# Kernel optimization log

Measured on AMD Instinct MI355X. Metric: run time of the kernel, lower is better.

Reference implementation:

```python
import jax, jax.numpy as jnp
import numpy as np

N, D, N_CLASSES = 4096, 256, 64
MARGIN = 0.2


def setup_inputs() -> dict:
    key = jax.random.key(0)
    k1, k2 = jax.random.split(key)
    embeddings = jax.random.normal(k1, (N, D), dtype=jnp.float32)
    labels = jax.random.randint(k2, (N,), 0, N_CLASSES)
    same = labels[:, None] == labels[None, :]
    eye = jnp.eye(N, dtype=bool)
    return {
        "embeddings": embeddings,
        "positives_mask": same & ~eye,
        "negatives_mask": ~same,
    }


def reference(embeddings, positives_mask, negatives_mask):
    # Pairwise squared L2 distances (LpDistance, normalize_embeddings=False)
    sq = jnp.sum(embeddings * embeddings, axis=1)  # [N]
    d2 = sq[:, None] + sq[None, :] - 2.0 * (embeddings @ embeddings.T)  # [N,N]
    d2 = jnp.maximum(d2, 0.0)

    # Batch-hard mining (argmax/argmin on squared dists == on L2 dists)
    hp = jnp.argmax(jnp.where(positives_mask, d2, -jnp.inf), axis=1)  # hardest positive per anchor
    hn = jnp.argmin(jnp.where(negatives_mask, d2, jnp.inf), axis=1)   # hardest negative per anchor
    rows = jnp.arange(N)

    d_ap = jnp.sqrt(d2[rows, hp])
    d_an = jnp.sqrt(d2[rows, hn])
    d_pn = jnp.sqrt(d2[hp, hn])

    # TripletMarginLoss with swap=True: use min(d(a,n), d(p,n))
    d_an_eff = jnp.minimum(d_an, d_pn)
    l = jax.nn.relu(d_ap - d_an_eff + MARGIN)  # [N] per-anchor triplet loss

    # Only anchors with >=1 positive and >=1 negative form valid triplets
    valid = jnp.any(positives_mask, axis=1) & jnp.any(negatives_mask, axis=1)
    nonzero = (l > 0) & valid
    cnt = jnp.sum(nonzero).astype(jnp.float32)
    total = jnp.sum(jnp.where(nonzero, l, 0.0))
    # AvgNonZeroReducer: mean over strictly-positive losses; 0 if none
    return jnp.where(cnt > 0, total / jnp.maximum(cnt, 1.0), 0.0)
```

## Files before the change

kernel.cpp:

```cpp
#include <hip/hip_runtime.h>
#include <math.h>


#define NN 4096
#define DD 256
#define MARGIN 0.2f
#define NCHUNK 32
#define BK 64

typedef _Float16 f16;
typedef __attribute__((ext_vector_type(8))) _Float16 f16x8;
typedef __attribute__((ext_vector_type(4))) _Float16 f16x4;
typedef __attribute__((ext_vector_type(4))) float f32x4;
typedef unsigned long long u64;
typedef unsigned int u32;

#define OFF_SQ     64
#define OFF_EH     (OFF_SQ + NN * 4)
#define OFF_POSB   (OFF_EH + NN * DD * 2)
#define OFF_PPK    (OFF_POSB + (NN * (long)NN / 8))
#define OFF_PNK    (OFF_PPK + NN * NCHUNK * 8)
#define OFF_LOSS   (OFF_PNK + NN * NCHUNK * 8)

#define CONV_BLOCKS   (NN / 4)
#define REPACK_BLOCKS 4096
#define PREP_BLOCKS   (CONV_BLOCKS + REPACK_BLOCKS)

__device__ __forceinline__ int swz(int r) { return (r ^ (r >> 3)) & 7; }

__device__ __forceinline__ void dma16(const void* g, void* l) {
  __builtin_amdgcn_global_load_lds(
      (const __attribute__((address_space(1))) void*)g,
      (__attribute__((address_space(3))) void*)l, 16, 0, 0);
}

__global__ __launch_bounds__(256)
void prep_kernel(const float* __restrict__ E, const void* __restrict__ pos_raw,
                 f16* __restrict__ Eh, float* __restrict__ sq,
                 u64* __restrict__ posb) {
  const int bid = blockIdx.x;
  const int tid = threadIdx.x;
  if (bid < CONV_BLOCKS) {
    const int row = bid * 4 + (tid >> 6);
    const int lane = tid & 63;
    const float4 v = *(const float4*)&E[(size_t)row * DD + lane * 4];
    f16x4 h;
    h[0] = (f16)v.x; h[1] = (f16)v.y; h[2] = (f16)v.z; h[3] = (f16)v.w;
    *(f16x4*)&Eh[(size_t)row * DD + lane * 4] = h;
    float s = v.x * v.x + v.y * v.y + v.z * v.z + v.w * v.w;
#pragma unroll
    for (int off = 32; off > 0; off >>= 1) s += __shfl_down(s, off);
    if (lane == 0) sq[row] = s;
    return;
  }

  __shared__ int s_ev[4];
  int ev = 0;
#pragma unroll
  for (int k = 0; k < 16; ++k) {
    const int di = tid + (k << 8);
    const u32 v = ((const u32*)pos_raw)[di];
    if (v & 0xffffff00u) ev |= 1;
    if (v == 0x3f800000u) ev |= 2;
    if (di & 1) {
      if (v == 0x3ff00000u) ev |= 4;
      if (v) ev |= 8;
    }
  }
#pragma unroll
  for (int off = 32; off > 0; off >>= 1) ev |= __shfl_xor(ev, off);
  if ((tid & 63) == 0) s_ev[tid >> 6] = ev;
  __syncthreads();
  ev = s_ev[0] | s_ev[1] | s_ev[2] | s_ev[3];
  int f;
  if (ev & 2) f = 2;
  else if (ev & 4) f = 4;
  else if (ev & 1) f = 1;
  else if (ev & 8) f = 0;
  else f = 3;

  const long long stride = (long long)REPACK_BLOCKS * 256;
  const long long base = (long long)(bid - CONV_BLOCKS) * 256 + tid;
#pragma unroll
  for (int it = 0; it < 16; ++it) {
    const long long idx = base + it * stride;
    bool p;
    if (f == 0)      p = ((const u32*)pos_raw)[idx] != 0u;
    else if (f == 1) p = ((const unsigned char*)pos_raw)[idx] != 0;
    else if (f == 2) p = ((const float*)pos_raw)[idx] != 0.f;
    else if (f == 3) p = ((const u64*)pos_raw)[idx] != 0ull;
    else             p = ((const double*)pos_raw)[idx] != 0.0;
    const u64 w = __ballot(p);
    if ((tid & 63) == 0) posb[idx >> 6] = w;
  }
}

__global__ __launch_bounds__(256)
void mine_kernel(const f16* __restrict__ Eh, const float* __restrict__ sq,
                 const u64* __restrict__ posb,
                 u64* __restrict__ part_p, u64* __restrict__ part_n) {
  __shared__ union {
    struct { f16 A[128 * BK]; f16 B[128 * BK]; } t;
    struct { u64 pk[2][128]; u64 nk[2][128]; } r;
  } sm;

  const int tid = threadIdx.x;
  const int lane = tid & 63, wave = tid >> 6;
  const int lx = lane & 15, q = lane >> 4;
  const int wr = wave >> 1, wc = wave & 1;
  const int ib = blockIdx.x & 31, jb = blockIdx.x >> 5;
  const int i0 = ib * 128, j0 = jb * 128;

  f32x4 acc[4][4];
#pragma unroll
  for (int mt = 0; mt < 4; ++mt)
#pragma unroll
    for (int nt = 0; nt < 4; ++nt) acc[mt][nt] = (f32x4)0.f;

  const int drow = lane >> 3;
  const int dslot = lane & 7;

  for (int kk = 0; kk < DD; kk += BK) {
    __syncthreads();
#pragma unroll
    for (int t = 0; t < 4; ++t) {
      const int i = wave * 4 + t;
      const int r = i * 8 + drow;
      const int g = dslot ^ swz(r);
      dma16(Eh + (size_t)(i0 + r) * DD + kk + g * 8, &sm.t.A[i * 512]);
      dma16(Eh + (size_t)(j0 + r) * DD + kk + g * 8, &sm.t.B[i * 512]);
    }
    __syncthreads();
#pragma unroll
    for (int ss = 0; ss < 2; ++ss) {
      f16x8 af[4], bf[4];
#pragma unroll
      for (int mt = 0; mt < 4; ++mt) {
        const int r = wr * 64 + mt * 16 + lx;
        af[mt] = *(const f16x8*)&sm.t.A[r * BK + (((ss * 4 + q) ^ swz(r)) << 3)];
      }
#pragma unroll
      for (int nt = 0; nt < 4; ++nt) {
        const int r = wc * 64 + nt * 16 + lx;
        bf[nt] = *(const f16x8*)&sm.t.B[r * BK + (((ss * 4 + q) ^ swz(r)) << 3)];
      }
#pragma unroll
      for (int mt = 0; mt < 4; ++mt)
#pragma unroll
        for (int nt = 0; nt < 4; ++nt)
          acc[mt][nt] = __builtin_amdgcn_mfma_f32_16x16x32_f16(bf[nt], af[mt], acc[mt][nt], 0, 0, 0);
    }
  }

  float sqi_[4];
  u64 pw_[4], nw_[4];
  const int jw = (j0 + wc * 64) >> 6;
#pragma unroll
  for (int mt = 0; mt < 4; ++mt) {
    const int gi = i0 + wr * 64 + mt * 16 + lx;
    sqi_[mt] = sq[gi];
    const u64 pw = posb[(size_t)gi * (NN / 64) + jw];
    const u64 eye = ((gi >> 6) == jw) ? (1ull << (gi & 63)) : 0ull;
    pw_[mt] = pw;
    nw_[mt] = ~(pw | eye);
  }
  f32x4 sqjv[4];
#pragma unroll
  for (int nt = 0; nt < 4; ++nt)
    sqjv[nt] = *(const f32x4*)&sq[j0 + wc * 64 + nt * 16 + q * 4];
  const u32 jlo_base = ~(u32)(j0 + wc * 64 + q * 4);

  u64 pk[4] = {0ull, 0ull, 0ull, 0ull};
  u64 nk[4] = {0ull, 0ull, 0ull, 0ull};
#pragma unroll
  for (int mt = 0; mt < 4; ++mt) {
#pragma unroll
    for (int nt = 0; nt < 4; ++nt) {
#pragma unroll
      for (int r = 0; r < 4; ++r) {
        const int c = nt * 16 + q * 4 + r;
        const float d2 = fmaxf(fmaf(-2.f, acc[mt][nt][r], sqi_[mt] + sqjv[nt][r]), 0.f);
        const u32 hi = __float_as_uint(d2);
        const u32 lo = jlo_base - (u32)(nt * 16 + r);
        const u64 key = ((u64)hi << 32) | lo;
        const u64 nkey = ((u64)(~hi) << 32) | lo;
        if ((pw_[mt] >> c) & 1ull) pk[mt] = key > pk[mt] ? key : pk[mt];
        if ((nw_[mt] >> c) & 1ull) nk[mt] = nkey > nk[mt] ? nkey : nk[mt];
      }
    }
  }
#pragma unroll
  for (int mt = 0; mt < 4; ++mt) {
#pragma unroll
    for (int off = 16; off < 64; off <<= 1) {
      u64 o = __shfl_xor(pk[mt], off);
      if (o > pk[mt]) pk[mt] = o;
      o = __shfl_xor(nk[mt], off);
      if (o > nk[mt]) nk[mt] = o;
    }
  }

  __syncthreads();
  if (q == 0) {
#pragma unroll
    for (int mt = 0; mt < 4; ++mt) {
      const int lr = wr * 64 + mt * 16 + lx;
      sm.r.pk[wc][lr] = pk[mt];
      sm.r.nk[wc][lr] = nk[mt];
    }
  }
  __syncthreads();
  if (tid < 128) {
    const u64 p0 = sm.r.pk[0][tid], p1 = sm.r.pk[1][tid];
    const u64 n0 = sm.r.nk[0][tid], n1 = sm.r.nk[1][tid];
    part_p[(size_t)jb * NN + i0 + tid] = p0 > p1 ? p0 : p1;
    part_n[(size_t)jb * NN + i0 + tid] = n0 > n1 ? n0 : n1;
  }
}

__global__ __launch_bounds__(256)
void finalize_kernel(const float* __restrict__ E, const float* __restrict__ sq,
                     const u64* __restrict__ part_p, const u64* __restrict__ part_n,
                     float* __restrict__ loss) {
  const int tid = threadIdx.x;
  const int a = blockIdx.x * 4 + (tid >> 6);
  const int lane = tid & 63;
  const int ch = lane & 31;
  u64 key = (lane < 32) ? part_p[(size_t)ch * NN + a] : part_n[(size_t)ch * NN + a];
#pragma unroll
  for (int off = 1; off < 32; off <<= 1) {
    const u64 o = __shfl_xor(key, off);
    if (o > key) key = o;
  }
  const u64 pkey = __shfl(key, 0);
  const u64 nkey = __shfl(key, 32);
  const bool valid = (pkey != 0ull) && (nkey != 0ull);
  const int p = (int)(~(u32)pkey);
  const int n = (int)(~(u32)nkey);
  const int pp = valid ? p : 0, nn = valid ? n : 0;

  const float4 xa = *(const float4*)&E[(size_t)a * DD + lane * 4];
  const float4 xp = *(const float4*)&E[(size_t)pp * DD + lane * 4];
  const float4 xn = *(const float4*)&E[(size_t)nn * DD + lane * 4];
  float dap = xa.x * xp.x + xa.y * xp.y + xa.z * xp.z + xa.w * xp.w;
  float dan = xa.x * xn.x + xa.y * xn.y + xa.z * xn.z + xa.w * xn.w;
  float dpn = xp.x * xn.x + xp.y * xn.y + xp.z * xn.z + xp.w * xn.w;
#pragma unroll
  for (int off = 32; off > 0; off >>= 1) {
    dap += __shfl_down(dap, off);
    dan += __shfl_down(dan, off);
    dpn += __shfl_down(dpn, off);
  }
  if (lane == 0) {
    float l = 0.f;
    if (valid) {
      const float d2ap = fmaxf(sq[a] + sq[pp] - 2.f * dap, 0.f);
      const float d2an = fmaxf(sq[a] + sq[nn] - 2.f * dan, 0.f);
      const float d2pn = fmaxf(sq[pp] + sq[nn] - 2.f * dpn, 0.f);
      l = fmaxf(sqrtf(d2ap) - fminf(sqrtf(d2an), sqrtf(d2pn)) + MARGIN, 0.f);
    }
    loss[a] = l;
  }
}

__global__ __launch_bounds__(1024)
void reduce_kernel(const float* __restrict__ loss, float* __restrict__ out) {
  __shared__ float s_sum[16], s_cnt[16];
  const int tid = threadIdx.x;
  const float4 v = *(const float4*)&loss[tid * 4];
  float s = v.x + v.y + v.z + v.w;
  float c = (v.x > 0.f) + (v.y > 0.f) + (v.z > 0.f) + (v.w > 0.f);
#pragma unroll
  for (int off = 32; off > 0; off >>= 1) {
    s += __shfl_down(s, off);
    c += __shfl_down(c, off);
  }
  if ((tid & 63) == 0) { s_sum[tid >> 6] = s; s_cnt[tid >> 6] = c; }
  __syncthreads();
  if (tid == 0) {
    float ts = 0.f, tc = 0.f;
#pragma unroll
    for (int w = 0; w < 16; ++w) { ts += s_sum[w]; tc += s_cnt[w]; }
    out[0] = (tc > 0.f) ? (ts / fmaxf(tc, 1.f)) : 0.f;
  }
}

extern "C" void kernel_launch(void* const* d_in, const int* in_sizes, int n_in,
                              void* d_out, int out_size, void* d_ws, size_t ws_size,
                              hipStream_t stream) {
  const float* E = (const float*)d_in[0];
  const void* posm = d_in[1];
  float* out = (float*)d_out;
  char* ws = (char*)d_ws;

  float* sq = (float*)(ws + OFF_SQ);
  f16* Eh = (f16*)(ws + OFF_EH);
  u64* posb = (u64*)(ws + OFF_POSB);
  u64* ppk = (u64*)(ws + OFF_PPK);
  u64* pnk = (u64*)(ws + OFF_PNK);
  float* loss = (float*)(ws + OFF_LOSS);

  prep_kernel<<<PREP_BLOCKS, 256, 0, stream>>>(E, posm, Eh, sq, posb);
  mine_kernel<<<32 * NCHUNK, 256, 0, stream>>>(Eh, sq, posb, ppk, pnk);
  finalize_kernel<<<NN / 4, 256, 0, stream>>>(E, sq, ppk, pnk, loss);
  reduce_kernel<<<1, 1024, 0, stream>>>(loss, out);
}
```

Measured before the change: 179.2 us.

## Load GEMM fragments directly from global memory instead of LDS staging

The mine kernel's Gram-matrix GEMM no longer stages 128x64 tiles of A and B into shared memory via global_load_lds with swizzling and barriers. Each wave now reads its MFMA operand fragments straight from global (L2/L1-cached) memory, with the K loop unrolled by two. This removes LDS traffic and the per-K-step barriers and cuts shared memory use, which may raise occupancy. In exchange, each wave issues redundant global loads, since sibling waves re-read the same rows, and it relies on cache hits for data reuse.

Measured after the change: 195.8 us. 9.3% more time.

```diff
diff --git a/kernel.cpp b/kernel.cpp
--- a/kernel.cpp
+++ b/kernel.cpp
@@ -6,7 +6,6 @@
 #define DD 256
 #define MARGIN 0.2f
 #define NCHUNK 32
-#define BK 64
 
 typedef _Float16 f16;
 typedef __attribute__((ext_vector_type(8))) _Float16 f16x8;
@@ -25,14 +24,6 @@
 #define CONV_BLOCKS   (NN / 4)
 #define REPACK_BLOCKS 4096
 #define PREP_BLOCKS   (CONV_BLOCKS + REPACK_BLOCKS)
-
-__device__ __forceinline__ int swz(int r) { return (r ^ (r >> 3)) & 7; }
-
-__device__ __forceinline__ void dma16(const void* g, void* l) {
-  __builtin_amdgcn_global_load_lds(
-      (const __attribute__((address_space(1))) void*)g,
-      (__attribute__((address_space(3))) void*)l, 16, 0, 0);
-}
 
 __global__ __launch_bounds__(256)
 void prep_kernel(const float* __restrict__ E, const void* __restrict__ pos_raw,
@@ -99,10 +90,7 @@
 void mine_kernel(const f16* __restrict__ Eh, const float* __restrict__ sq,
                  const u64* __restrict__ posb,
                  u64* __restrict__ part_p, u64* __restrict__ part_n) {
-  __shared__ union {
-    struct { f16 A[128 * BK]; f16 B[128 * BK]; } t;
-    struct { u64 pk[2][128]; u64 nk[2][128]; } r;
-  } sm;
+  __shared__ u64 s_pk[2][128], s_nk[2][128];
 
   const int tid = threadIdx.x;
   const int lane = tid & 63, wave = tid >> 6;
@@ -117,39 +105,28 @@
 #pragma unroll
     for (int nt = 0; nt < 4; ++nt) acc[mt][nt] = (f32x4)0.f;
 
-  const int drow = lane >> 3;
-  const int dslot = lane & 7;
-
-  for (int kk = 0; kk < DD; kk += BK) {
-    __syncthreads();
-#pragma unroll
-    for (int t = 0; t < 4; ++t) {
-      const int i = wave * 4 + t;
-      const int r = i * 8 + drow;
-      const int g = dslot ^ swz(r);
-      dma16(Eh + (size_t)(i0 + r) * DD + kk + g * 8, &sm.t.A[i * 512]);
-      dma16(Eh + (size_t)(j0 + r) * DD + kk + g * 8, &sm.t.B[i * 512]);
-    }
-    __syncthreads();
-#pragma unroll
-    for (int ss = 0; ss < 2; ++ss) {
-      f16x8 af[4], bf[4];
-#pragma unroll
-      for (int mt = 0; mt < 4; ++mt) {
-        const int r = wr * 64 + mt * 16 + lx;
-        af[mt] = *(const f16x8*)&sm.t.A[r * BK + (((ss * 4 + q) ^ swz(r)) << 3)];
-      }
-#pragma unroll
-      for (int nt = 0; nt < 4; ++nt) {
-        const int r = wc * 64 + nt * 16 + lx;
-        bf[nt] = *(const f16x8*)&sm.t.B[r * BK + (((ss * 4 + q) ^ swz(r)) << 3)];
-      }
-#pragma unroll
-      for (int mt = 0; mt < 4; ++mt)
-#pragma unroll
-        for (int nt = 0; nt < 4; ++nt)
-          acc[mt][nt] = __builtin_amdgcn_mfma_f32_16x16x32_f16(bf[nt], af[mt], acc[mt][nt], 0, 0, 0);
-    }
+  const f16* abase[4];
+  const f16* bbase[4];
+#pragma unroll
+  for (int mt = 0; mt < 4; ++mt)
+    abase[mt] = Eh + (size_t)(i0 + wr * 64 + mt * 16 + lx) * DD + q * 8;
+#pragma unroll
+  for (int nt = 0; nt < 4; ++nt)
+    bbase[nt] = Eh + (size_t)(j0 + wc * 64 + nt * 16 + lx) * DD + q * 8;
+
+#pragma unroll 2
+  for (int ks = 0; ks < DD / 32; ++ks) {
+    const int col = ks * 32;
+    f16x8 af[4], bf[4];
+#pragma unroll
+    for (int mt = 0; mt < 4; ++mt) af[mt] = *(const f16x8*)(abase[mt] + col);
+#pragma unroll
+    for (int nt = 0; nt < 4; ++nt) bf[nt] = *(const f16x8*)(bbase[nt] + col);
+#pragma unroll
+    for (int mt = 0; mt < 4; ++mt)
+#pragma unroll
+      for (int nt = 0; nt < 4; ++nt)
+        acc[mt][nt] = __builtin_amdgcn_mfma_f32_16x16x32_f16(bf[nt], af[mt], acc[mt][nt], 0, 0, 0);
   }
 
   float sqi_[4];
@@ -200,19 +177,18 @@
     }
   }
 
-  __syncthreads();
   if (q == 0) {
 #pragma unroll
     for (int mt = 0; mt < 4; ++mt) {
       const int lr = wr * 64 + mt * 16 + lx;
-      sm.r.pk[wc][lr] = pk[mt];
-      sm.r.nk[wc][lr] = nk[mt];
+      s_pk[wc][lr] = pk[mt];
+      s_nk[wc][lr] = nk[mt];
     }
   }
   __syncthreads();
   if (tid < 128) {
-    const u64 p0 = sm.r.pk[0][tid], p1 = sm.r.pk[1][tid];
-    const u64 n0 = sm.r.nk[0][tid], n1 = sm.r.nk[1][tid];
+    const u64 p0 = s_pk[0][tid], p1 = s_pk[1][tid];
+    const u64 n0 = s_nk[0][tid], n1 = s_nk[1][tid];
     part_p[(size_t)jb * NN + i0 + tid] = p0 > p1 ? p0 : p1;
     part_n[(size_t)jb * NN + i0 + tid] = n0 > n1 ? n0 : n1;
   }
```
